# Optimization experiments

Hardware: AMD Instinct MI355X
Metric: run time of the kernel (lower is better)

Reference implementation:

```python
import jax, jax.numpy as jnp
import numpy as np

B, S, N, D = 4, 96, 512, 8
H = 64
OUT = 24
TARGET_NODE = 0


def setup_inputs() -> dict:
    key = jax.random.key(0)
    ks = jax.random.split(key, 8)
    x = jax.random.normal(ks[0], (B, S, N, D), dtype=jnp.float32)
    adj = jax.random.uniform(ks[1], (B, S, N, N), dtype=jnp.float32) / N  # row-normalized-ish
    h0 = jnp.zeros((B, N, H), dtype=jnp.float32)
    c0 = jnp.zeros((B, N, H), dtype=jnp.float32)
    Wx = jax.random.normal(ks[2], (D, 4 * H), dtype=jnp.float32) * (1.0 / np.sqrt(D))
    Wh = jax.random.normal(ks[3], (H, 4 * H), dtype=jnp.float32) * (1.0 / np.sqrt(H))
    b_gates = jnp.zeros((4 * H,), dtype=jnp.float32)
    W1 = jax.random.normal(ks[4], (H, H // 2), dtype=jnp.float32) * (1.0 / np.sqrt(H))
    b1 = jnp.zeros((H // 2,), dtype=jnp.float32)
    W2 = jax.random.normal(ks[5], (H // 2, OUT), dtype=jnp.float32) * (1.0 / np.sqrt(H // 2))
    b2 = jnp.zeros((OUT,), dtype=jnp.float32)
    return {"x": x, "adj": adj, "initial_hidden_state": h0, "initial_cell_state": c0,
            "Wx": Wx, "Wh": Wh, "b_gates": b_gates, "W1": W1, "b1": b1, "W2": W2, "b2": b2}


def reference(x, adj, initial_hidden_state, initial_cell_state, Wx, Wh, b_gates, W1, b1, W2, b2):
    # GCLSTM: per-timestep graph conv fused into LSTM gate equations.
    def step(carry, inp):
        h, c = carry
        xt, at = inp  # xt: (B,N,D), at: (B,N,N)
        # graph conv on input and hidden, then project to 4 gates
        gx = jnp.einsum('bnm,bmd->bnd', at, xt) @ Wx   # (B,N,4H)
        gh = jnp.einsum('bnm,bmh->bnh', at, h) @ Wh    # (B,N,4H)
        g = gx + gh + b_gates
        i, f, o, gg = jnp.split(g, 4, axis=-1)
        i = jax.nn.sigmoid(i)
        f = jax.nn.sigmoid(f)
        o = jax.nn.sigmoid(o)
        gg = jnp.tanh(gg)
        c_new = f * c + i * gg
        h_new = o * jnp.tanh(c_new)
        return (h_new, c_new), None

    xs = jnp.swapaxes(x, 0, 1)      # (S,B,N,D)
    adjs = jnp.swapaxes(adj, 0, 1)  # (S,B,N,N)
    (h, c), _ = jax.lax.scan(step, (initial_hidden_state, initial_cell_state), (xs, adjs))
    read_out = h[:, TARGET_NODE, :]                    # (B,H)
    out = jax.nn.relu(read_out @ W1 + b1) @ W2 + b2    # (B,OUT)
    return out
```

## Files before the change

### kernel.cpp

```cpp
#include <hip/hip_runtime.h>
#include <math.h>

#define BB   4
#define SS   96
#define NN   512
#define DD   8
#define HH   64
#define G4   256
#define OUTK 24

#define THREADS 512
#define NBLK    256
#define RPB     8
#define AST     580
#define AHWS    516
#define CSTR    64
#define BARSZ   (BB * CSTR)

typedef float f32x4 __attribute__((ext_vector_type(4)));

__global__ void bar_init(unsigned* __restrict__ bar) {
    const int i = blockIdx.x * 256 + threadIdx.x;
    if (i < BARSZ) bar[i] = 0u;
}

__device__ __forceinline__ float sigm_f(float v) { return 1.f / (1.f + __expf(-v)); }
__device__ __forceinline__ float tanh_f(float v) { return 1.f - 2.f / (__expf(2.f * v) + 1.f); }

__device__ __forceinline__ void vfma(f32x4& d, float s, f32x4 v) {
    d.x = fmaf(s, v.x, d.x); d.y = fmaf(s, v.y, d.y);
    d.z = fmaf(s, v.z, d.z); d.w = fmaf(s, v.w, d.w);
}

__global__ __launch_bounds__(THREADS, 2) void gnn_lstm_persist(
    const float* __restrict__ x,
    const float* __restrict__ adj,
    const float* __restrict__ h0,
    const float* __restrict__ c0,
    const float* __restrict__ Wx,
    const float* __restrict__ Wh,
    const float* __restrict__ bg,
    const float* __restrict__ W1, const float* __restrict__ b1,
    const float* __restrict__ W2, const float* __restrict__ b2,
    float* __restrict__ out,
    float* __restrict__ hA, float* __restrict__ hB,
    unsigned* __restrict__ bar)
{
    __shared__ float a_lds[RPB * AST];
    __shared__ float x_lds[NN * DD];
    __shared__ float u_lds[8 * AHWS];
    __shared__ float ax_part[THREADS];
    __shared__ float ah_lds[RPB * HH];
    __shared__ float ax_s[RPB * DD];
    __shared__ float hh_s[HH];
    __shared__ float z1_s[32];

    const int tid  = threadIdx.x;
    const int bid  = blockIdx.x;
    const int b    = bid >> 6;
    const int slot = bid & 63;
    const int n0   = slot * RPB;
    const int r_g  = tid >> 6;
    const int j_g  = tid & 63;

    unsigned* const broot = bar + b * CSTR;

    const int half = tid >> 8;
    const int jj   = tid & 255;
    float whcol[36];
    if (half == 0) {
        #pragma unroll
        for (int k = 0; k < 36; ++k) whcol[k] = Wh[k * G4 + jj];
    } else {
        #pragma unroll
        for (int k = 0; k < 28; ++k) whcol[k] = Wh[(36 + k) * G4 + jj];
        #pragma unroll
        for (int d = 0; d < 8; ++d)  whcol[28 + d] = Wx[d * G4 + jj];
    }
    const float bias = (half == 0) ? bg[jj] : 0.f;
    const size_t sidx = ((size_t)b * NN + n0 + r_g) * HH + j_g;
    float c_reg = c0[sidx];

    {
        const float* ab = adj + (((size_t)b * SS + 0) * NN + n0) * NN;
        const float* xb = x + ((size_t)b * SS + 0) * (NN * DD);
        f32x4 pa0 = *(const f32x4*)(ab + tid * 4);
        f32x4 pa1 = *(const f32x4*)(ab + 2048 + tid * 4);
        f32x4 px0 = *(const f32x4*)(xb + tid * 4);
        f32x4 px1 = *(const f32x4*)(xb + 2048 + tid * 4);
        const int f0 = tid * 4;
        *(f32x4*)(a_lds + (f0 >> 9) * AST + (f0 & 511)) = pa0;
        const int f1 = 2048 + tid * 4;
        *(f32x4*)(a_lds + (f1 >> 9) * AST + (f1 & 511)) = pa1;
        *(f32x4*)(x_lds + tid * 4) = px0;
        *(f32x4*)(x_lds + 2048 + tid * 4) = px1;
    }
    __syncthreads();

    f32x4 qa0, qa1, qx0, qx1;
    {
        const float* ab = adj + (((size_t)b * SS + 1) * NN + n0) * NN;
        const float* xb = x + ((size_t)b * SS + 1) * (NN * DD);
        qa0 = *(const f32x4*)(ab + tid * 4);
        qa1 = *(const f32x4*)(ab + 2048 + tid * 4);
        qx0 = *(const f32x4*)(xb + tid * 4);
        qx1 = *(const f32x4*)(xb + 2048 + tid * 4);
    }

    {
        const int d = tid & 7, rr = (tid >> 3) & 7, mg2 = tid >> 6;
        const float* ar = a_lds + rr * AST + mg2 * 64;
        const float* xr = x_lds + mg2 * 512 + d;
        float s = 0.f;
        #pragma unroll
        for (int mi = 0; mi < 64; ++mi) s = fmaf(ar[mi], xr[mi * 8], s);
        ax_part[tid] = s;
    }

    const float* hp = h0;
    float* hd = hB;

    const int c4 = (tid & 15) * 4;
    const int m0 = (tid >> 4) * 16;

    for (int t = 0; t < SS; ++t) {
        f32x4 hv[16];
        {
            const float* hpb = hp + (size_t)b * NN * HH;
            const unsigned long long hbase =
                (unsigned long long)(const void*)(hpb + (size_t)m0 * HH + c4);
#define HLOAD(I, OFFS) \
            asm volatile("global_load_dwordx4 %0, %1, off offset:" OFFS " sc0 sc1" \
                         : "=v"(hv[I]) : "v"(hbase) : "memory")
            HLOAD(0, "0");     HLOAD(1, "256");   HLOAD(2, "512");   HLOAD(3, "768");
            HLOAD(4, "1024");  HLOAD(5, "1280");  HLOAD(6, "1536");  HLOAD(7, "1792");
            HLOAD(8, "2048");  HLOAD(9, "2304");  HLOAD(10, "2560"); HLOAD(11, "2816");
            HLOAD(12, "3072"); HLOAD(13, "3328"); HLOAD(14, "3584"); HLOAD(15, "3840");
#undef HLOAD
        }
        {
            f32x4 acc[8];
            #pragma unroll
            for (int r = 0; r < 8; ++r) acc[r] = f32x4{0.f, 0.f, 0.f, 0.f};
#define AH_CHUNK(MI4) \
            { \
                _Pragma("unroll") \
                for (int r = 0; r < 8; ++r) { \
                    const f32x4 a4 = *(const f32x4*)(a_lds + r * AST + m0 + (MI4)); \
                    vfma(acc[r], a4.x, hv[(MI4) + 0]); \
                    vfma(acc[r], a4.y, hv[(MI4) + 1]); \
                    vfma(acc[r], a4.z, hv[(MI4) + 2]); \
                    vfma(acc[r], a4.w, hv[(MI4) + 3]); \
                } \
            }
            asm volatile("s_waitcnt vmcnt(12)" ::: "memory");
            __builtin_amdgcn_sched_barrier(0);
            AH_CHUNK(0)
            asm volatile("s_waitcnt vmcnt(8)" ::: "memory");
            __builtin_amdgcn_sched_barrier(0);
            AH_CHUNK(4)
            asm volatile("s_waitcnt vmcnt(4)" ::: "memory");
            __builtin_amdgcn_sched_barrier(0);
            AH_CHUNK(8)
            asm volatile("s_waitcnt vmcnt(0)" ::: "memory");
            __builtin_amdgcn_sched_barrier(0);
            AH_CHUNK(12)
#undef AH_CHUNK
            #pragma unroll
            for (int r = 0; r < 8; ++r) {
                acc[r].x += __shfl_xor(acc[r].x, 16); acc[r].y += __shfl_xor(acc[r].y, 16);
                acc[r].z += __shfl_xor(acc[r].z, 16); acc[r].w += __shfl_xor(acc[r].w, 16);
                acc[r].x += __shfl_xor(acc[r].x, 32); acc[r].y += __shfl_xor(acc[r].y, 32);
                acc[r].z += __shfl_xor(acc[r].z, 32); acc[r].w += __shfl_xor(acc[r].w, 32);
            }
            if ((tid & 48) == 0) {
                const int w = tid >> 6;
                #pragma unroll
                for (int r = 0; r < 8; ++r)
                    *(f32x4*)(u_lds + w * AHWS + r * 64 + c4) = acc[r];
            }
        }
        __syncthreads();

        {
            float s = 0.f;
            #pragma unroll
            for (int w2 = 0; w2 < 8; ++w2) s += u_lds[w2 * AHWS + tid];
            ah_lds[tid] = s;
            if (tid < 64) {
                float s2 = 0.f;
                #pragma unroll
                for (int w2 = 0; w2 < 8; ++w2) s2 += ax_part[w2 * 64 + tid];
                ax_s[tid] = s2;
            }
        }
        __syncthreads();

        {
            float g[8];
            #pragma unroll
            for (int r = 0; r < 8; ++r) g[r] = bias;
            if (half == 0) {
                #pragma unroll
                for (int k4 = 0; k4 < 36; k4 += 4) {
                    #pragma unroll
                    for (int r = 0; r < 8; ++r) {
                        const f32x4 a4 = *(const f32x4*)(ah_lds + r * 64 + k4);
                        g[r] = fmaf(a4.x, whcol[k4 + 0], g[r]);
                        g[r] = fmaf(a4.y, whcol[k4 + 1], g[r]);
                        g[r] = fmaf(a4.z, whcol[k4 + 2], g[r]);
                        g[r] = fmaf(a4.w, whcol[k4 + 3], g[r]);
                    }
                }
            } else {
                #pragma unroll
                for (int k4 = 0; k4 < 28; k4 += 4) {
                    #pragma unroll
                    for (int r = 0; r < 8; ++r) {
                        const f32x4 a4 = *(const f32x4*)(ah_lds + r * 64 + 36 + k4);
                        g[r] = fmaf(a4.x, whcol[k4 + 0], g[r]);
                        g[r] = fmaf(a4.y, whcol[k4 + 1], g[r]);
                        g[r] = fmaf(a4.z, whcol[k4 + 2], g[r]);
                        g[r] = fmaf(a4.w, whcol[k4 + 3], g[r]);
                    }
                }
                #pragma unroll
                for (int d4 = 0; d4 < 8; d4 += 4) {
                    #pragma unroll
                    for (int r = 0; r < 8; ++r) {
                        const f32x4 a4 = *(const f32x4*)(ax_s + r * 8 + d4);
                        g[r] = fmaf(a4.x, whcol[28 + d4 + 0], g[r]);
                        g[r] = fmaf(a4.y, whcol[28 + d4 + 1], g[r]);
                        g[r] = fmaf(a4.z, whcol[28 + d4 + 2], g[r]);
                        g[r] = fmaf(a4.w, whcol[28 + d4 + 3], g[r]);
                    }
                }
            }
            #pragma unroll
            for (int r = 0; r < 8; ++r) u_lds[(half * 8 + r) * 256 + jj] = g[r];
        }
        __syncthreads();

        float hn;
        {
            const float gi = u_lds[r_g * 256 + j_g]       + u_lds[(8 + r_g) * 256 + j_g];
            const float gf = u_lds[r_g * 256 + 64 + j_g]  + u_lds[(8 + r_g) * 256 + 64 + j_g];
            const float go = u_lds[r_g * 256 + 128 + j_g] + u_lds[(8 + r_g) * 256 + 128 + j_g];
            const float gg = u_lds[r_g * 256 + 192 + j_g] + u_lds[(8 + r_g) * 256 + 192 + j_g];
            const float ig = sigm_f(gi);
            const float fg = sigm_f(gf);
            const float og = sigm_f(go);
            const float gt = tanh_f(gg);
            c_reg = fg * c_reg + ig * gt;
            hn = og * tanh_f(c_reg);
        }
        if (t == SS - 1) {
            if (slot == 0 && tid < 64) hh_s[tid] = hn;
            break;
        }
        {
            const unsigned long long haddr = (unsigned long long)(const void*)(hd + sidx);
            asm volatile("global_store_dword %0, %1, off sc0 sc1"
                         :: "v"(haddr), "v"(hn) : "memory");
        }

        {
            const int f0 = tid * 4;
            *(f32x4*)(a_lds + (f0 >> 9) * AST + (f0 & 511)) = qa0;
            const int f1 = 2048 + tid * 4;
            *(f32x4*)(a_lds + (f1 >> 9) * AST + (f1 & 511)) = qa1;
            *(f32x4*)(x_lds + tid * 4) = qx0;
            *(f32x4*)(x_lds + 2048 + tid * 4) = qx1;
        }
        asm volatile("s_waitcnt vmcnt(0)" ::: "memory");
        __syncthreads();

        if (tid == 0)
            __hip_atomic_fetch_add(broot, 1u, __ATOMIC_RELAXED, __HIP_MEMORY_SCOPE_AGENT);

        {
            const int t2 = (t + 2 < SS) ? t + 2 : SS - 1;
            const float* ab = adj + (((size_t)b * SS + t2) * NN + n0) * NN;
            const float* xb = x + ((size_t)b * SS + t2) * (NN * DD);
            qa0 = *(const f32x4*)(ab + tid * 4);
            qa1 = *(const f32x4*)(ab + 2048 + tid * 4);
            qx0 = *(const f32x4*)(xb + tid * 4);
            qx1 = *(const f32x4*)(xb + 2048 + tid * 4);
        }

        {
            const int d = tid & 7, rr = (tid >> 3) & 7, mg2 = tid >> 6;
            const float* ar = a_lds + rr * AST + mg2 * 64;
            const float* xr = x_lds + mg2 * 512 + d;
            float s = 0.f;
            #pragma unroll
            for (int mi = 0; mi < 64; ++mi) s = fmaf(ar[mi], xr[mi * 8], s);
            ax_part[tid] = s;
        }

        if (tid == 0) {
            const unsigned tgt = 64u * (unsigned)(t + 1);
            while (__hip_atomic_load(broot, __ATOMIC_RELAXED, __HIP_MEMORY_SCOPE_AGENT) < tgt)
                __builtin_amdgcn_s_sleep(1);
        }
        __syncthreads();
        __builtin_amdgcn_sched_barrier(0);

        hp = hd;
        hd = (hd == hA) ? hB : hA;
    }

    if (slot == 0) {
        __syncthreads();
        if (tid < 32) {
            float s = b1[tid];
            #pragma unroll
            for (int j = 0; j < 64; ++j) s = fmaf(hh_s[j], W1[j * 32 + tid], s);
            z1_s[tid] = fmaxf(s, 0.f);
        }
        __syncthreads();
        if (tid < OUTK) {
            float s = b2[tid];
            #pragma unroll
            for (int k = 0; k < 32; ++k) s = fmaf(z1_s[k], W2[k * 24 + tid], s);
            out[b * OUTK + tid] = s;
        }
    }
}

extern "C" void kernel_launch(void* const* d_in, const int* in_sizes, int n_in,
                              void* d_out, int out_size, void* d_ws, size_t ws_size,
                              hipStream_t stream) {
    const float* x   = (const float*)d_in[0];
    const float* adj = (const float*)d_in[1];
    const float* h0  = (const float*)d_in[2];
    const float* c0  = (const float*)d_in[3];
    const float* Wx  = (const float*)d_in[4];
    const float* Wh  = (const float*)d_in[5];
    const float* bg  = (const float*)d_in[6];
    const float* W1  = (const float*)d_in[7];
    const float* b1  = (const float*)d_in[8];
    const float* W2  = (const float*)d_in[9];
    const float* b2  = (const float*)d_in[10];
    float* out = (float*)d_out;

    const int NE = BB * NN * HH;
    float* ws = (float*)d_ws;
    float* hA = ws;
    float* hB = ws + NE;
    unsigned* bar = (unsigned*)(ws + 2 * NE);

    bar_init<<<(BARSZ + 255) / 256, 256, 0, stream>>>(bar);

    void* args[] = { (void*)&x, (void*)&adj, (void*)&h0, (void*)&c0,
                     (void*)&Wx, (void*)&Wh, (void*)&bg,
                     (void*)&W1, (void*)&b1, (void*)&W2, (void*)&b2,
                     (void*)&out, (void*)&hA, (void*)&hB, (void*)&bar };
    hipLaunchCooperativeKernel((void*)gnn_lstm_persist,
                               dim3(NBLK), dim3(THREADS), args, 0, stream);
}
```

Baseline: 806.9 us.

## Template rows-per-block and launch 512 blocks with 4 rows each

Turns the persistent cooperative kernel into a template over rows per block and adds a 4-row variant. That variant launches twice as many blocks (512 instead of 256) and sets launch bounds to 4 blocks per CU, and the host checks occupancy to choose between the two. The aim is to spread the per-timestep recurrent work over more CUs and cut per-block latency on the serial time chain. The cost is more blocks to join at each grid-wide barrier, more redundant x/h loads per block, and idle threads in some phases.

```diff
diff --git a/kernel.cpp b/kernel.cpp
--- a/kernel.cpp
+++ b/kernel.cpp
@@ -10,8 +10,6 @@
 #define OUTK 24
 
 #define THREADS 512
-#define NBLK    256
-#define RPB     8
 #define AST     580
 #define AHWS    516
 #define CSTR    64
@@ -32,7 +30,8 @@
     d.z = fmaf(s, v.z, d.z); d.w = fmaf(s, v.w, d.w);
 }
 
-__global__ __launch_bounds__(THREADS, 2) void gnn_lstm_persist(
+template<int RPB>
+__global__ __launch_bounds__(THREADS, 4) void gnn_lstm_persist(
     const float* __restrict__ x,
     const float* __restrict__ adj,
     const float* __restrict__ h0,
@@ -46,6 +45,11 @@
     float* __restrict__ hA, float* __restrict__ hB,
     unsigned* __restrict__ bar)
 {
+    constexpr int BPB  = NN / RPB;
+    constexpr int PGRP = 8 * RPB;
+    constexpr int NCH  = THREADS / PGRP;
+    constexpr int MPC  = NN / NCH;
+
     __shared__ float a_lds[RPB * AST];
     __shared__ float x_lds[NN * DD];
     __shared__ float u_lds[8 * AHWS];
@@ -57,10 +61,10 @@
 
     const int tid  = threadIdx.x;
     const int bid  = blockIdx.x;
-    const int b    = bid >> 6;
-    const int slot = bid & 63;
+    const int b    = bid / BPB;
+    const int slot = bid % BPB;
     const int n0   = slot * RPB;
-    const int r_g  = tid >> 6;
+    const int r_g  = (tid >> 6) & (RPB - 1);
     const int j_g  = tid & 63;
 
     unsigned* const broot = bar + b * CSTR;
@@ -85,13 +89,15 @@
         const float* ab = adj + (((size_t)b * SS + 0) * NN + n0) * NN;
         const float* xb = x + ((size_t)b * SS + 0) * (NN * DD);
         f32x4 pa0 = *(const f32x4*)(ab + tid * 4);
-        f32x4 pa1 = *(const f32x4*)(ab + 2048 + tid * 4);
         f32x4 px0 = *(const f32x4*)(xb + tid * 4);
         f32x4 px1 = *(const f32x4*)(xb + 2048 + tid * 4);
         const int f0 = tid * 4;
         *(f32x4*)(a_lds + (f0 >> 9) * AST + (f0 & 511)) = pa0;
-        const int f1 = 2048 + tid * 4;
-        *(f32x4*)(a_lds + (f1 >> 9) * AST + (f1 & 511)) = pa1;
+        if constexpr (RPB == 8) {
+            f32x4 pa1 = *(const f32x4*)(ab + 2048 + tid * 4);
+            const int f1 = 2048 + tid * 4;
+            *(f32x4*)(a_lds + (f1 >> 9) * AST + (f1 & 511)) = pa1;
+        }
         *(f32x4*)(x_lds + tid * 4) = px0;
         *(f32x4*)(x_lds + 2048 + tid * 4) = px1;
     }
@@ -102,18 +108,18 @@
         const float* ab = adj + (((size_t)b * SS + 1) * NN + n0) * NN;
         const float* xb = x + ((size_t)b * SS + 1) * (NN * DD);
         qa0 = *(const f32x4*)(ab + tid * 4);
-        qa1 = *(const f32x4*)(ab + 2048 + tid * 4);
+        if constexpr (RPB == 8) qa1 = *(const f32x4*)(ab + 2048 + tid * 4);
         qx0 = *(const f32x4*)(xb + tid * 4);
         qx1 = *(const f32x4*)(xb + 2048 + tid * 4);
     }
 
     {
-        const int d = tid & 7, rr = (tid >> 3) & 7, mg2 = tid >> 6;
-        const float* ar = a_lds + rr * AST + mg2 * 64;
-        const float* xr = x_lds + mg2 * 512 + d;
+        const int d = tid & 7, rr = (tid >> 3) & (RPB - 1), mg2 = tid / PGRP;
+        const float* ar = a_lds + rr * AST + mg2 * MPC;
+        const float* xr = x_lds + mg2 * MPC * DD + d;
         float s = 0.f;
         #pragma unroll
-        for (int mi = 0; mi < 64; ++mi) s = fmaf(ar[mi], xr[mi * 8], s);
+        for (int mi = 0; mi < MPC; ++mi) s = fmaf(ar[mi], xr[mi * 8], s);
         ax_part[tid] = s;
     }
 
@@ -139,13 +145,13 @@
 #undef HLOAD
         }
         {
-            f32x4 acc[8];
-            #pragma unroll
-            for (int r = 0; r < 8; ++r) acc[r] = f32x4{0.f, 0.f, 0.f, 0.f};
+            f32x4 acc[RPB];
+            #pragma unroll
+            for (int r = 0; r < RPB; ++r) acc[r] = f32x4{0.f, 0.f, 0.f, 0.f};
 #define AH_CHUNK(MI4) \
             { \
                 _Pragma("unroll") \
-                for (int r = 0; r < 8; ++r) { \
+                for (int r = 0; r < RPB; ++r) { \
                     const f32x4 a4 = *(const f32x4*)(a_lds + r * AST + m0 + (MI4)); \
                     vfma(acc[r], a4.x, hv[(MI4) + 0]); \
                     vfma(acc[r], a4.y, hv[(MI4) + 1]); \
@@ -167,7 +173,7 @@
             AH_CHUNK(12)
 #undef AH_CHUNK
             #pragma unroll
-            for (int r = 0; r < 8; ++r) {
+            for (int r = 0; r < RPB; ++r) {
                 acc[r].x += __shfl_xor(acc[r].x, 16); acc[r].y += __shfl_xor(acc[r].y, 16);
                 acc[r].z += __shfl_xor(acc[r].z, 16); acc[r].w += __shfl_xor(acc[r].w, 16);
                 acc[r].x += __shfl_xor(acc[r].x, 32); acc[r].y += __shfl_xor(acc[r].y, 32);
@@ -176,35 +182,37 @@
             if ((tid & 48) == 0) {
                 const int w = tid >> 6;
                 #pragma unroll
-                for (int r = 0; r < 8; ++r)
+                for (int r = 0; r < RPB; ++r)
                     *(f32x4*)(u_lds + w * AHWS + r * 64 + c4) = acc[r];
             }
         }
         __syncthreads();
 
         {
-            float s = 0.f;
-            #pragma unroll
-            for (int w2 = 0; w2 < 8; ++w2) s += u_lds[w2 * AHWS + tid];
-            ah_lds[tid] = s;
-            if (tid < 64) {
+            if (tid < RPB * HH) {
+                float s = 0.f;
+                #pragma unroll
+                for (int w2 = 0; w2 < 8; ++w2) s += u_lds[w2 * AHWS + tid];
+                ah_lds[tid] = s;
+            }
+            if (tid < PGRP) {
                 float s2 = 0.f;
                 #pragma unroll
-                for (int w2 = 0; w2 < 8; ++w2) s2 += ax_part[w2 * 64 + tid];
+                for (int c2 = 0; c2 < NCH; ++c2) s2 += ax_part[c2 * PGRP + tid];
                 ax_s[tid] = s2;
             }
         }
         __syncthreads();
 
         {
-            float g[8];
-            #pragma unroll
-            for (int r = 0; r < 8; ++r) g[r] = bias;
+            float g[RPB];
+            #pragma unroll
+            for (int r = 0; r < RPB; ++r) g[r] = bias;
             if (half == 0) {
                 #pragma unroll
                 for (int k4 = 0; k4 < 36; k4 += 4) {
                     #pragma unroll
-                    for (int r = 0; r < 8; ++r) {
+                    for (int r = 0; r < RPB; ++r) {
                         const f32x4 a4 = *(const f32x4*)(ah_lds + r * 64 + k4);
                         g[r] = fmaf(a4.x, whcol[k4 + 0], g[r]);
                         g[r] = fmaf(a4.y, whcol[k4 + 1], g[r]);
@@ -216,7 +224,7 @@
                 #pragma unroll
                 for (int k4 = 0; k4 < 28; k4 += 4) {
                     #pragma unroll
-                    for (int r = 0; r < 8; ++r) {
+                    for (int r = 0; r < RPB; ++r) {
                         const f32x4 a4 = *(const f32x4*)(ah_lds + r * 64 + 36 + k4);
                         g[r] = fmaf(a4.x, whcol[k4 + 0], g[r]);
                         g[r] = fmaf(a4.y, whcol[k4 + 1], g[r]);
@@ -227,7 +235,7 @@
                 #pragma unroll
                 for (int d4 = 0; d4 < 8; d4 += 4) {
                     #pragma unroll
-                    for (int r = 0; r < 8; ++r) {
+                    for (int r = 0; r < RPB; ++r) {
                         const f32x4 a4 = *(const f32x4*)(ax_s + r * 8 + d4);
                         g[r] = fmaf(a4.x, whcol[28 + d4 + 0], g[r]);
                         g[r] = fmaf(a4.y, whcol[28 + d4 + 1], g[r]);
@@ -237,16 +245,16 @@
                 }
             }
             #pragma unroll
-            for (int r = 0; r < 8; ++r) u_lds[(half * 8 + r) * 256 + jj] = g[r];
+            for (int r = 0; r < RPB; ++r) u_lds[(half * RPB + r) * 256 + jj] = g[r];
         }
         __syncthreads();
 
         float hn;
         {
-            const float gi = u_lds[r_g * 256 + j_g]       + u_lds[(8 + r_g) * 256 + j_g];
-            const float gf = u_lds[r_g * 256 + 64 + j_g]  + u_lds[(8 + r_g) * 256 + 64 + j_g];
-            const float go = u_lds[r_g * 256 + 128 + j_g] + u_lds[(8 + r_g) * 256 + 128 + j_g];
-            const float gg = u_lds[r_g * 256 + 192 + j_g] + u_lds[(8 + r_g) * 256 + 192 + j_g];
+            const float gi = u_lds[r_g * 256 + j_g]       + u_lds[(RPB + r_g) * 256 + j_g];
+            const float gf = u_lds[r_g * 256 + 64 + j_g]  + u_lds[(RPB + r_g) * 256 + 64 + j_g];
+            const float go = u_lds[r_g * 256 + 128 + j_g] + u_lds[(RPB + r_g) * 256 + 128 + j_g];
+            const float gg = u_lds[r_g * 256 + 192 + j_g] + u_lds[(RPB + r_g) * 256 + 192 + j_g];
             const float ig = sigm_f(gi);
             const float fg = sigm_f(gf);
             const float og = sigm_f(go);
@@ -258,7 +266,7 @@
             if (slot == 0 && tid < 64) hh_s[tid] = hn;
             break;
         }
-        {
+        if ((tid >> 6) < RPB) {
             const unsigned long long haddr = (unsigned long long)(const void*)(hd + sidx);
             asm volatile("global_store_dword %0, %1, off sc0 sc1"
                          :: "v"(haddr), "v"(hn) : "memory");
@@ -267,8 +275,10 @@
         {
             const int f0 = tid * 4;
             *(f32x4*)(a_lds + (f0 >> 9) * AST + (f0 & 511)) = qa0;
-            const int f1 = 2048 + tid * 4;
-            *(f32x4*)(a_lds + (f1 >> 9) * AST + (f1 & 511)) = qa1;
+            if constexpr (RPB == 8) {
+                const int f1 = 2048 + tid * 4;
+                *(f32x4*)(a_lds + (f1 >> 9) * AST + (f1 & 511)) = qa1;
+            }
             *(f32x4*)(x_lds + tid * 4) = qx0;
             *(f32x4*)(x_lds + 2048 + tid * 4) = qx1;
         }
@@ -283,23 +293,23 @@
             const float* ab = adj + (((size_t)b * SS + t2) * NN + n0) * NN;
             const float* xb = x + ((size_t)b * SS + t2) * (NN * DD);
             qa0 = *(const f32x4*)(ab + tid * 4);
-            qa1 = *(const f32x4*)(ab + 2048 + tid * 4);
+            if constexpr (RPB == 8) qa1 = *(const f32x4*)(ab + 2048 + tid * 4);
             qx0 = *(const f32x4*)(xb + tid * 4);
             qx1 = *(const f32x4*)(xb + 2048 + tid * 4);
         }
 
         {
-            const int d = tid & 7, rr = (tid >> 3) & 7, mg2 = tid >> 6;
-            const float* ar = a_lds + rr * AST + mg2 * 64;
-            const float* xr = x_lds + mg2 * 512 + d;
+            const int d = tid & 7, rr = (tid >> 3) & (RPB - 1), mg2 = tid / PGRP;
+            const float* ar = a_lds + rr * AST + mg2 * MPC;
+            const float* xr = x_lds + mg2 * MPC * DD + d;
             float s = 0.f;
             #pragma unroll
-            for (int mi = 0; mi < 64; ++mi) s = fmaf(ar[mi], xr[mi * 8], s);
+            for (int mi = 0; mi < MPC; ++mi) s = fmaf(ar[mi], xr[mi * 8], s);
             ax_part[tid] = s;
         }
 
         if (tid == 0) {
-            const unsigned tgt = 64u * (unsigned)(t + 1);
+            const unsigned tgt = (unsigned)BPB * (unsigned)(t + 1);
             while (__hip_atomic_load(broot, __ATOMIC_RELAXED, __HIP_MEMORY_SCOPE_AGENT) < tgt)
                 __builtin_amdgcn_s_sleep(1);
         }
@@ -350,12 +360,29 @@
     float* hB = ws + NE;
     unsigned* bar = (unsigned*)(ws + 2 * NE);
 
-    bar_init<<<(BARSZ + 255) / 256, 256, 0, stream>>>(bar);
+    bar_init<<<1, 256, 0, stream>>>(bar);
 
     void* args[] = { (void*)&x, (void*)&adj, (void*)&h0, (void*)&c0,
                      (void*)&Wx, (void*)&Wh, (void*)&bg,
                      (void*)&W1, (void*)&b1, (void*)&W2, (void*)&b2,
                      (void*)&out, (void*)&hA, (void*)&hB, (void*)&bar };
-    hipLaunchCooperativeKernel((void*)gnn_lstm_persist,
-                               dim3(NBLK), dim3(THREADS), args, 0, stream);
+
+    static int occ4 = -1;
+    if (occ4 < 0) {
+        int n = 0;
+        if (hipOccupancyMaxActiveBlocksPerMultiprocessor(
+                &n, reinterpret_cast<const void*>(gnn_lstm_persist<4>),
+                THREADS, 0) != hipSuccess)
+            n = 0;
+        occ4 = n;
+    }
+    if (occ4 >= 2) {
+        (void)hipLaunchCooperativeKernel((void*)gnn_lstm_persist<4>,
+                                         dim3(BB * (NN / 4)), dim3(THREADS),
+                                         args, 0, stream);
+    } else {
+        (void)hipLaunchCooperativeKernel((void*)gnn_lstm_persist<8>,
+                                         dim3(BB * (NN / 8)), dim3(THREADS),
+                                         args, 0, stream);
+    }
 }
```

After: 1.896 ms. 2.35x slower.

## Replace atomic-counter grid barrier with per-block flags polled per wavefront

Applied to the files above, without the earlier changes.

Each block now posts its step number to its own padded flag slot instead of incrementing a shared per-batch counter. Every wavefront polls the flags of the eight producer blocks whose h rows it will read, then loads them, so the block-wide spin and __syncthreads at the end of each step are removed. The h loads are also split into two halves with a full wait between them, which lowers live registers but serialises part of the load latency. The risk is more polling traffic, plus correctness depending on relaxed flag stores being ordered after the h stores.

```diff
diff --git a/kernel.cpp b/kernel.cpp
--- a/kernel.cpp
+++ b/kernel.cpp
@@ -14,8 +14,9 @@
 #define RPB     8
 #define AST     580
 #define AHWS    516
-#define CSTR    64
-#define BARSZ   (BB * CSTR)
+#define FSLOT   16
+#define FSTR    (64 * FSLOT)
+#define BARSZ   (BB * FSTR)
 
 typedef float f32x4 __attribute__((ext_vector_type(4)));
 
@@ -63,7 +64,11 @@
     const int r_g  = tid >> 6;
     const int j_g  = tid & 63;
 
-    unsigned* const broot = bar + b * CSTR;
+    unsigned* const pfb    = bar + b * FSTR;
+    const int pw           = ((tid >> 6) << 3) + (tid & 7);
+    unsigned* const fwatch = pfb + pw * FSLOT;
+    unsigned* const fpost  = pfb + slot * FSLOT;
+    const bool selfw       = (pw == slot);
 
     const int half = tid >> 8;
     const int jj   = tid & 255;
@@ -124,47 +129,58 @@
     const int m0 = (tid >> 4) * 16;
 
     for (int t = 0; t < SS; ++t) {
-        f32x4 hv[16];
+        if (t) {
+            for (;;) {
+                unsigned fv = __hip_atomic_load(fwatch, __ATOMIC_RELAXED,
+                                                __HIP_MEMORY_SCOPE_AGENT);
+                if (selfw) fv = (unsigned)t;
+                if (__all(fv >= (unsigned)t)) break;
+                __builtin_amdgcn_s_sleep(1);
+            }
+            __builtin_amdgcn_sched_barrier(0);
+        }
+
+        f32x4 hv[8], hw[8];
         {
             const float* hpb = hp + (size_t)b * NN * HH;
             const unsigned long long hbase =
                 (unsigned long long)(const void*)(hpb + (size_t)m0 * HH + c4);
-#define HLOAD(I, OFFS) \
+#define HLV(I, OFFS) \
             asm volatile("global_load_dwordx4 %0, %1, off offset:" OFFS " sc0 sc1" \
                          : "=v"(hv[I]) : "v"(hbase) : "memory")
-            HLOAD(0, "0");     HLOAD(1, "256");   HLOAD(2, "512");   HLOAD(3, "768");
-            HLOAD(4, "1024");  HLOAD(5, "1280");  HLOAD(6, "1536");  HLOAD(7, "1792");
-            HLOAD(8, "2048");  HLOAD(9, "2304");  HLOAD(10, "2560"); HLOAD(11, "2816");
-            HLOAD(12, "3072"); HLOAD(13, "3328"); HLOAD(14, "3584"); HLOAD(15, "3840");
-#undef HLOAD
+#define HLW(I, OFFS) \
+            asm volatile("global_load_dwordx4 %0, %1, off offset:" OFFS " sc0 sc1" \
+                         : "=v"(hw[I]) : "v"(hbase) : "memory")
+            HLV(0, "0");    HLV(1, "256");  HLV(2, "512");  HLV(3, "768");
+            HLV(4, "1024"); HLV(5, "1280"); HLV(6, "1536"); HLV(7, "1792");
+            asm volatile("s_waitcnt vmcnt(0)" ::: "memory");
+            __builtin_amdgcn_sched_barrier(0);
+            HLW(0, "2048"); HLW(1, "2304"); HLW(2, "2560"); HLW(3, "2816");
+            HLW(4, "3072"); HLW(5, "3328"); HLW(6, "3584"); HLW(7, "3840");
+#undef HLV
+#undef HLW
         }
         {
             f32x4 acc[8];
             #pragma unroll
             for (int r = 0; r < 8; ++r) acc[r] = f32x4{0.f, 0.f, 0.f, 0.f};
-#define AH_CHUNK(MI4) \
+#define AH_CHUNK(ARR, MI4, BASE) \
             { \
                 _Pragma("unroll") \
                 for (int r = 0; r < 8; ++r) { \
                     const f32x4 a4 = *(const f32x4*)(a_lds + r * AST + m0 + (MI4)); \
-                    vfma(acc[r], a4.x, hv[(MI4) + 0]); \
-                    vfma(acc[r], a4.y, hv[(MI4) + 1]); \
-                    vfma(acc[r], a4.z, hv[(MI4) + 2]); \
-                    vfma(acc[r], a4.w, hv[(MI4) + 3]); \
+                    vfma(acc[r], a4.x, ARR[(MI4) - (BASE) + 0]); \
+                    vfma(acc[r], a4.y, ARR[(MI4) - (BASE) + 1]); \
+                    vfma(acc[r], a4.z, ARR[(MI4) - (BASE) + 2]); \
+                    vfma(acc[r], a4.w, ARR[(MI4) - (BASE) + 3]); \
                 } \
             }
-            asm volatile("s_waitcnt vmcnt(12)" ::: "memory");
-            __builtin_amdgcn_sched_barrier(0);
-            AH_CHUNK(0)
-            asm volatile("s_waitcnt vmcnt(8)" ::: "memory");
-            __builtin_amdgcn_sched_barrier(0);
-            AH_CHUNK(4)
-            asm volatile("s_waitcnt vmcnt(4)" ::: "memory");
-            __builtin_amdgcn_sched_barrier(0);
-            AH_CHUNK(8)
+            AH_CHUNK(hv, 0, 0)
+            AH_CHUNK(hv, 4, 0)
             asm volatile("s_waitcnt vmcnt(0)" ::: "memory");
             __builtin_amdgcn_sched_barrier(0);
-            AH_CHUNK(12)
+            AH_CHUNK(hw, 8, 8)
+            AH_CHUNK(hw, 12, 8)
 #undef AH_CHUNK
             #pragma unroll
             for (int r = 0; r < 8; ++r) {
@@ -276,7 +292,8 @@
         __syncthreads();
 
         if (tid == 0)
-            __hip_atomic_fetch_add(broot, 1u, __ATOMIC_RELAXED, __HIP_MEMORY_SCOPE_AGENT);
+            __hip_atomic_store(fpost, (unsigned)(t + 1), __ATOMIC_RELAXED,
+                               __HIP_MEMORY_SCOPE_AGENT);
 
         {
             const int t2 = (t + 2 < SS) ? t + 2 : SS - 1;
@@ -297,14 +314,6 @@
             for (int mi = 0; mi < 64; ++mi) s = fmaf(ar[mi], xr[mi * 8], s);
             ax_part[tid] = s;
         }
-
-        if (tid == 0) {
-            const unsigned tgt = 64u * (unsigned)(t + 1);
-            while (__hip_atomic_load(broot, __ATOMIC_RELAXED, __HIP_MEMORY_SCOPE_AGENT) < tgt)
-                __builtin_amdgcn_s_sleep(1);
-        }
-        __syncthreads();
-        __builtin_amdgcn_sched_barrier(0);
 
         hp = hd;
         hd = (hd == hA) ? hB : hA;
```

After: 740.1 us. 1.09x faster.
